# Performance work log

Measured on AMD Instinct MI355X. Metric: run time of the kernel, lower is better.

## Reference

```python
import jax, jax.numpy as jnp
from jax import lax
import numpy as np

T = 8  # num_temp_tokens (init kwarg, closed over as a static constant)


def setup_inputs() -> dict:
    key = jax.random.key(0)
    k1, k2, k3, k4, k5 = jax.random.split(key, 5)
    B, N, C = 16, 197, 768
    bt = B * T
    x = jax.random.normal(k1, (bt, N, C), dtype=jnp.float32)
    # routing conv1d: C -> 3C, kernel 3 (original inits to zero; small random for testing)
    a_weight = jax.random.normal(k2, (3 * C, C, 3), dtype=jnp.float32) * 0.02
    a_bias = jax.random.normal(k3, (3 * C,), dtype=jnp.float32) * 0.02
    # main linear weight (out_channels=3C, in_channels=C) and bias
    weight = jax.random.normal(k4, (3 * C, C), dtype=jnp.float32) * 0.02
    bias = jax.random.normal(k5, (3 * C,), dtype=jnp.float32) * 0.02
    return {"x": x, "a_weight": a_weight, "a_bias": a_bias, "weight": weight, "bias": bias}


def reference(x, a_weight, a_bias, weight, bias):
    bt, n, c = x.shape
    b = bt // T
    xr = x.reshape(b, T, n, c)                      # (b, t, n, c)
    # routing: conv1d over T on the CLS token, then +1
    cls = jnp.transpose(xr[:, :, 0, :], (0, 2, 1))  # (b, c, t)
    r = lax.conv_general_dilated(
        cls, a_weight, window_strides=(1,), padding=[(1, 1)],
        dimension_numbers=("NCH", "OIH", "NCH"),
    ) + a_bias[None, :, None] + 1.0                 # (b, 3c, t)
    s = jnp.transpose(r, (0, 2, 1)).reshape(b, T, 3, c)   # per-(b,t) q/k/v c_in scales
    Wr = weight.reshape(3, c, c)                    # (3, c_out, c_in)
    br = bias.reshape(3, c)
    # scale input channels per (b, t, group), then batched GEMM
    xs = xr[:, :, None, :, :] * s[:, :, :, None, :]       # (b, t, 3, n, c)
    out = jnp.einsum("goi,btgni->btgon", Wr, xs)          # (b, t, 3, c_out, n)
    out = out + (br[None, None] * s)[..., None]           # bias also modulated by scales
    return out.reshape(bt, 3 * c, n)                # (b*t, 3c, n) == torch output layout
```

## Files before the change

kernel.cpp:

```cpp
#include <hip/hip_runtime.h>

#define NTOK 197
#define C 768
#define C3 2304
#define BK 32
#define PK 40
#define NT 13
#define CPAD 772
#define AWP 200

typedef __attribute__((ext_vector_type(4))) float f32x4;
typedef __attribute__((ext_vector_type(8))) short bf16x8;
typedef unsigned int u32;

__device__ __forceinline__ ushort f2bf(float f){
  uint u = __float_as_uint(f);
  u += 0x7fffu + ((u >> 16) & 1u);
  return (ushort)(u >> 16);
}
__device__ __forceinline__ uint pack2(float a, float b){
  return (uint)f2bf(a) | ((uint)f2bf(b) << 16);
}
__device__ __forceinline__ float bfu2f(uint u){ return __uint_as_float(u << 16); }

__device__ __forceinline__ void glds16(ushort* lds, const ushort* gsrc){
  __builtin_amdgcn_global_load_lds((const __attribute__((address_space(1))) u32*)gsrc,
                                   (__attribute__((address_space(3))) u32*)lds, 16, 0, 0);
}

#define N4_W 442368
#define N4_X 4841472
__global__ __launch_bounds__(256)
void cvt_all(const float* __restrict__ w, const float* __restrict__ x,
             ushort* __restrict__ wbf, ushort* __restrict__ xbf)
{
  const int tid0 = blockIdx.x*256 + threadIdx.x;
  const int stride = gridDim.x*256;
  for (int i = tid0; i < N4_W; i += stride){
    float4 v = reinterpret_cast<const float4*>(w)[i];
    ushort4 o; o.x=f2bf(v.x); o.y=f2bf(v.y); o.z=f2bf(v.z); o.w=f2bf(v.w);
    reinterpret_cast<ushort4*>(wbf)[i] = o;
  }
  for (int i = tid0; i < N4_X; i += stride){
    float4 v = reinterpret_cast<const float4*>(x)[i];
    ushort4 o; o.x=f2bf(v.x); o.y=f2bf(v.y); o.z=f2bf(v.z); o.w=f2bf(v.w);
    reinterpret_cast<ushort4*>(xbf)[i] = o;
  }
}

__global__ __launch_bounds__(256)
void conv_part(const float* __restrict__ x, const float* __restrict__ aw,
               float* __restrict__ partial)
{
  __shared__ __align__(16) float  cls[16][10][68];
  __shared__ __align__(16) ushort awt[64*64*4];
  const int oc = blockIdx.x, kp = blockIdx.y, tid = threadIdx.x;
  const int k0 = kp*64;

  for (int task = tid; task < 2560; task += 256){
    int b = task / 160, rem = task % 160;
    int tp = rem / 16, c4 = rem % 16;
    float4 v = {0.f,0.f,0.f,0.f};
    if (tp >= 1 && tp <= 8)
      v = *reinterpret_cast<const float4*>(x + (size_t)(b*8 + tp - 1)*NTOK*C + k0 + c4*4);
    *reinterpret_cast<float4*>(&cls[b][tp][c4*4]) = v;
  }
  for (int task = tid; task < 1024; task += 256){
    int r = task >> 4, kc = task & 15;
    const float* p = aw + (size_t)(oc*64 + r)*2304 + (size_t)(k0 + kc*4)*3;
    float4 f0 = *reinterpret_cast<const float4*>(p);
    float4 f1 = *reinterpret_cast<const float4*>(p+4);
    float4 f2 = *reinterpret_cast<const float4*>(p+8);
    float f[12] = {f0.x,f0.y,f0.z,f0.w, f1.x,f1.y,f1.z,f1.w, f2.x,f2.y,f2.z,f2.w};
    uint4 o0, o1;
    o0.x = pack2(f[0], f[1]);  o0.y = (uint)f2bf(f[2]);
    o0.z = pack2(f[3], f[4]);  o0.w = (uint)f2bf(f[5]);
    o1.x = pack2(f[6], f[7]);  o1.y = (uint)f2bf(f[8]);
    o1.z = pack2(f[9], f[10]); o1.w = (uint)f2bf(f[11]);
    uint4* dst = reinterpret_cast<uint4*>(&awt[(r*64 + kc*4)*4]);
    dst[0] = o0; dst[1] = o1;
  }
  __syncthreads();

  const int o_l = tid >> 2, bq = tid & 3;
  float acc[8][4];
  #pragma unroll
  for (int t=0;t<8;t++)
    #pragma unroll
    for (int bi=0;bi<4;bi++) acc[t][bi]=0.f;

  #pragma unroll 1
  for (int kc = 0; kc < 16; ++kc){
    const uint4* ap = reinterpret_cast<const uint4*>(&awt[(o_l*64 + kc*4)*4]);
    uint4 aw0 = ap[0], aw1 = ap[1];
    float wv[4][3];
    wv[0][0]=bfu2f(aw0.x&0xffffu); wv[0][1]=bfu2f(aw0.x>>16); wv[0][2]=bfu2f(aw0.y&0xffffu);
    wv[1][0]=bfu2f(aw0.z&0xffffu); wv[1][1]=bfu2f(aw0.z>>16); wv[1][2]=bfu2f(aw0.w&0xffffu);
    wv[2][0]=bfu2f(aw1.x&0xffffu); wv[2][1]=bfu2f(aw1.x>>16); wv[2][2]=bfu2f(aw1.y&0xffffu);
    wv[3][0]=bfu2f(aw1.z&0xffffu); wv[3][1]=bfu2f(aw1.z>>16); wv[3][2]=bfu2f(aw1.w&0xffffu);
    #pragma unroll
    for (int bi=0; bi<4; ++bi){
      const int b = bq + 4*bi;
      float4 cv[10];
      #pragma unroll
      for (int tp=0; tp<10; tp++)
        cv[tp] = *reinterpret_cast<const float4*>(&cls[b][tp][kc*4]);
      #pragma unroll
      for (int t=0;t<8;t++){
        #pragma unroll
        for (int dk=0;dk<3;dk++){
          const float* cp = reinterpret_cast<const float*>(&cv[t+dk]);
          #pragma unroll
          for (int e=0;e<4;e++)
            acc[t][bi] += wv[e][dk] * cp[e];
        }
      }
    }
  }

  #pragma unroll
  for (int bi=0;bi<4;bi++){
    const int b = bq + 4*bi;
    #pragma unroll
    for (int t=0;t<8;t++)
      partial[((size_t)kp*128 + b*8 + t)*C3 + oc*64 + o_l] = acc[t][bi];
  }
}

__global__ __launch_bounds__(256)
void conv_reduce(const float* __restrict__ partial, const float* __restrict__ ab,
                 float* __restrict__ s_ws)
{
  const int o  = blockIdx.x*256 + threadIdx.x;
  const int bt = blockIdx.y;
  float v = ab[o] + 1.0f;
  #pragma unroll
  for (int kp=0; kp<12; kp++)
    v += partial[((size_t)kp*128 + bt)*C3 + o];
  s_ws[(size_t)bt*C3 + o] = v;
}

__global__ __launch_bounds__(256)
void gemm4(const ushort* __restrict__ wbf, const ushort* __restrict__ xbf,
           const float* __restrict__ s_ws, const float* __restrict__ bias,
           float* __restrict__ out)
{
  __shared__ __align__(16) ushort A_lds[2][128*BK];
  __shared__ __align__(16) ushort B_lds[2][208*BK];

  const int lid  = blockIdx.x;
  const int work = (lid & 7)*288 + (lid >> 3);
  const int bt   = work / 18;
  const int rem  = work - bt*18;
  const int g    = rem / 6;
  const int mt   = rem - g*6;

  const int tid = threadIdx.x, w = tid >> 6, lane = tid & 63;
  const int l15 = lane & 15, lq = lane >> 4;

  const float*  srow = s_ws + (size_t)bt*C3 + (size_t)g*C;
  const ushort* Ap   = wbf + ((size_t)g*C + (size_t)mt*128)*C;
  const ushort* xb   = xbf + (size_t)bt*NTOK*C;

  const int arow = tid >> 1;
  const int acol = (tid & 1) * 16;
  const ushort* awp = Ap + (size_t)arow*C + acol;
  const float*  asp = srow + acol;
  const int brow = lane >> 2;
  const int bcol = (lane & 3) * 8;

  f32x4 acc[2][13];
  #pragma unroll
  for (int i=0;i<2;i++)
    #pragma unroll
    for (int j=0;j<13;j++) acc[i][j] = (f32x4){0.f,0.f,0.f,0.f};

  {
    uint4 w0 = *reinterpret_cast<const uint4*>(awp);
    uint4 w1 = *reinterpret_cast<const uint4*>(awp + 8);
    float4 s0 = *reinterpret_cast<const float4*>(asp);
    float4 s1 = *reinterpret_cast<const float4*>(asp+4);
    float4 s2 = *reinterpret_cast<const float4*>(asp+8);
    float4 s3 = *reinterpret_cast<const float4*>(asp+12);
    for (int e = w; e < 13; e += 4)
      glds16(&B_lds[0][e*512], xb + (size_t)(e*16 + brow)*C + bcol);
    uint4 o0, o1;
    o0.x = pack2(bfu2f(w0.x&0xffffu)*s0.x, bfu2f(w0.x>>16)*s0.y);
    o0.y = pack2(bfu2f(w0.y&0xffffu)*s0.z, bfu2f(w0.y>>16)*s0.w);
    o0.z = pack2(bfu2f(w0.z&0xffffu)*s1.x, bfu2f(w0.z>>16)*s1.y);
    o0.w = pack2(bfu2f(w0.w&0xffffu)*s1.z, bfu2f(w0.w>>16)*s1.w);
    o1.x = pack2(bfu2f(w1.x&0xffffu)*s2.x, bfu2f(w1.x>>16)*s2.y);
    o1.y = pack2(bfu2f(w1.y&0xffffu)*s2.z, bfu2f(w1.y>>16)*s2.w);
    o1.z = pack2(bfu2f(w1.z&0xffffu)*s3.x, bfu2f(w1.z>>16)*s3.y);
    o1.w = pack2(bfu2f(w1.w&0xffffu)*s3.z, bfu2f(w1.w>>16)*s3.w);
    *reinterpret_cast<uint4*>(&A_lds[0][arow*BK + acol    ]) = o0;
    *reinterpret_cast<uint4*>(&A_lds[0][arow*BK + acol + 8]) = o1;
  }
  __syncthreads();

  for (int t = 0; t < 24; ++t){
    const int cur = t & 1, nxt = cur ^ 1;
    const int kn = t*BK + BK;
    uint4 w0, w1; float4 s0, s1, s2, s3;
    if (t < 23){
      w0 = *reinterpret_cast<const uint4*>(awp + kn);
      w1 = *reinterpret_cast<const uint4*>(awp + kn + 8);
      s0 = *reinterpret_cast<const float4*>(asp + kn);
      s1 = *reinterpret_cast<const float4*>(asp + kn + 4);
      s2 = *reinterpret_cast<const float4*>(asp + kn + 8);
      s3 = *reinterpret_cast<const float4*>(asp + kn + 12);
      for (int e = w; e < 13; e += 4)
        glds16(&B_lds[nxt][e*512], xb + (size_t)(e*16 + brow)*C + kn + bcol);
    }

    bf16x8 a0 = *reinterpret_cast<const bf16x8*>(&A_lds[cur][(w*32      + l15)*BK + lq*8]);
    bf16x8 a1 = *reinterpret_cast<const bf16x8*>(&A_lds[cur][(w*32 + 16 + l15)*BK + lq*8]);
    #pragma unroll
    for (int nf=0; nf<13; nf++){
      bf16x8 b = *reinterpret_cast<const bf16x8*>(&B_lds[cur][(nf*16 + l15)*BK + lq*8]);
      acc[0][nf] = __builtin_amdgcn_mfma_f32_16x16x32_bf16(a0, b, acc[0][nf], 0, 0, 0);
      acc[1][nf] = __builtin_amdgcn_mfma_f32_16x16x32_bf16(a1, b, acc[1][nf], 0, 0, 0);
    }

    if (t < 23){
      uint4 o0, o1;
      o0.x = pack2(bfu2f(w0.x&0xffffu)*s0.x, bfu2f(w0.x>>16)*s0.y);
      o0.y = pack2(bfu2f(w0.y&0xffffu)*s0.z, bfu2f(w0.y>>16)*s0.w);
      o0.z = pack2(bfu2f(w0.z&0xffffu)*s1.x, bfu2f(w0.z>>16)*s1.y);
      o0.w = pack2(bfu2f(w0.w&0xffffu)*s1.z, bfu2f(w0.w>>16)*s1.w);
      o1.x = pack2(bfu2f(w1.x&0xffffu)*s2.x, bfu2f(w1.x>>16)*s2.y);
      o1.y = pack2(bfu2f(w1.y&0xffffu)*s2.z, bfu2f(w1.y>>16)*s2.w);
      o1.z = pack2(bfu2f(w1.z&0xffffu)*s3.x, bfu2f(w1.z>>16)*s3.y);
      o1.w = pack2(bfu2f(w1.w&0xffffu)*s3.z, bfu2f(w1.w>>16)*s3.w);
      *reinterpret_cast<uint4*>(&A_lds[nxt][arow*BK + acol    ]) = o0;
      *reinterpret_cast<uint4*>(&A_lds[nxt][arow*BK + acol + 8]) = o1;
      __syncthreads();
    }
  }

  #pragma unroll
  for (int mf=0; mf<2; mf++){
    const int o0 = mt*128 + w*32 + mf*16 + lq*4;
    float bs[4];
    #pragma unroll
    for (int r=0;r<4;r++)
      bs[r] = bias[g*C + o0 + r] * srow[o0 + r];
    #pragma unroll
    for (int nf=0; nf<13; nf++){
      int n = nf*16 + l15;
      if (n < NTOK){
        #pragma unroll
        for (int r=0;r<4;r++)
          out[((size_t)bt*C3 + g*C + o0 + r)*NTOK + n] = acc[mf][nf][r] + bs[r];
      }
    }
  }
}

__global__ __launch_bounds__(256)
void conv3(const float* __restrict__ x, const float* __restrict__ aw,
           const float* __restrict__ ab, float* __restrict__ s_ws)
{
  __shared__ __align__(16) float  cls[10][CPAD];
  __shared__ __align__(16) ushort awt[64*AWP];
  __shared__ float partial[64][4][9];
  const int oc = blockIdx.x, b = blockIdx.y, tid = threadIdx.x;

  for (int task = tid; task < 1920; task += 256){
    int row = task / 192, c4 = task % 192;
    float4 v = {0.f,0.f,0.f,0.f};
    if (row >= 1 && row <= 8)
      v = *reinterpret_cast<const float4*>(x + (size_t)(b*8 + row - 1)*NTOK*C + c4*4);
    *reinterpret_cast<float4*>(&cls[row][c4*4]) = v;
  }

  const int o_l = tid >> 2, part = tid & 3;
  float acc[8];
  #pragma unroll
  for (int t=0;t<8;t++) acc[t]=0.f;

  for (int it = 0; it < 12; ++it){
    const int i0 = it*64;
    #pragma unroll
    for (int j = 0; j < 12; ++j){
      int task = tid + j*256;
      int r = task / 48, c4 = task % 48;
      float4 v = *reinterpret_cast<const float4*>(aw + (size_t)(oc*64 + r)*C3 + i0*3 + c4*4);
      uint2 pk; pk.x = pack2(v.x, v.y); pk.y = pack2(v.z, v.w);
      *reinterpret_cast<uint2*>(&awt[r*AWP + c4*4]) = pk;
    }
    __syncthreads();

    #pragma unroll
    for (int qq = 0; qq < 4; ++qq){
      const int i_loc = part*16 + qq*4;
      const int ib = i0 + i_loc;
      float4 cv[10];
      #pragma unroll
      for (int t=0;t<10;t++) cv[t] = *reinterpret_cast<const float4*>(&cls[t][ib]);
      float wv[4][3];
      #pragma unroll
      for (int e=0;e<4;e++){
        #pragma unroll
        for (int dk=0;dk<3;dk++)
          wv[e][dk] = bfu2f((uint)awt[o_l*AWP + (i_loc+e)*3 + dk]);
      }
      #pragma unroll
      for (int e=0;e<4;e++){
        #pragma unroll
        for (int dk=0;dk<3;dk++){
          const float wf = wv[e][dk];
          #pragma unroll
          for (int t=0;t<8;t++){
            const float* cp = reinterpret_cast<const float*>(&cv[t+dk]);
            acc[t] += wf * cp[e];
          }
        }
      }
    }
    __syncthreads();
  }

  #pragma unroll
  for (int t=0;t<8;t++) partial[o_l][part][t] = acc[t];
  __syncthreads();

  for (int idx = tid; idx < 512; idx += 256){
    int o = idx >> 3, t = idx & 7;
    float v = partial[o][0][t] + partial[o][1][t]
            + partial[o][2][t] + partial[o][3][t]
            + ab[oc*64 + o] + 1.0f;
    s_ws[(size_t)(b*8 + t)*C3 + oc*64 + o] = v;
  }
}

__global__ __launch_bounds__(512)
void gemm_fb(const float* __restrict__ x, const ushort* __restrict__ wbf,
             const float* __restrict__ s_ws, const float* __restrict__ bias,
             float* __restrict__ out)
{
  __shared__ __align__(16) ushort A_lds[128*PK];
  __shared__ __align__(16) ushort B_lds[208*PK];
  const int ot  = blockIdx.x;
  const int g   = blockIdx.y;
  const int bt  = blockIdx.z;
  const int tid = threadIdx.x;
  const int w = tid >> 6, lane = tid & 63;
  const int l15 = lane & 15, lq = lane >> 4;

  const float*  srow  = s_ws + (size_t)bt*C3 + (size_t)g*C;
  const ushort* wrow  = wbf + ((size_t)g*C + (size_t)ot*128)*C;
  const float*  xrow  = x   + (size_t)bt*NTOK*C;

  f32x4 acc[NT];
  #pragma unroll
  for (int j=0;j<NT;j++) acc[j] = (f32x4){0.f,0.f,0.f,0.f};

  const int ar = tid >> 2, ac = tid & 3;

  for (int k0 = 0; k0 < C; k0 += BK){
    {
      uint4 wv = *reinterpret_cast<const uint4*>(wrow + (size_t)ar*C + k0 + ac*8);
      const float* sv = srow + k0 + ac*8;
      float4 s0 = *reinterpret_cast<const float4*>(sv);
      float4 s1 = *reinterpret_cast<const float4*>(sv+4);
      uint4 av;
      av.x = pack2(bfu2f(wv.x & 0xffffu)*s0.x, bfu2f(wv.x >> 16)*s0.y);
      av.y = pack2(bfu2f(wv.y & 0xffffu)*s0.z, bfu2f(wv.y >> 16)*s0.w);
      av.z = pack2(bfu2f(wv.z & 0xffffu)*s1.x, bfu2f(wv.z >> 16)*s1.y);
      av.w = pack2(bfu2f(wv.w & 0xffffu)*s1.z, bfu2f(wv.w >> 16)*s1.w);
      *reinterpret_cast<uint4*>(&A_lds[ar*PK + ac*8]) = av;
    }
    #pragma unroll
    for (int it = 0; it < 2; ++it){
      int task = tid + it*512;
      if (task < 832){
        int r = task >> 2, cc = task & 3;
        uint4 bv = {0u,0u,0u,0u};
        if (r < NTOK){
          const float* p = xrow + (size_t)r*C + k0 + cc*8;
          float4 lo = *reinterpret_cast<const float4*>(p);
          float4 hi = *reinterpret_cast<const float4*>(p+4);
          bv.x = pack2(lo.x, lo.y); bv.y = pack2(lo.z, lo.w);
          bv.z = pack2(hi.x, hi.y); bv.w = pack2(hi.z, hi.w);
        }
        *reinterpret_cast<uint4*>(&B_lds[r*PK + cc*8]) = bv;
      }
    }
    __syncthreads();

    bf16x8 a = *reinterpret_cast<const bf16x8*>(&A_lds[(w*16 + l15)*PK + lq*8]);
    #pragma unroll
    for (int j=0;j<NT;j++){
      bf16x8 b = *reinterpret_cast<const bf16x8*>(&B_lds[(j*16 + l15)*PK + lq*8]);
      acc[j] = __builtin_amdgcn_mfma_f32_16x16x32_bf16(a, b, acc[j], 0, 0, 0);
    }
    __syncthreads();
  }

  const int obase = ot*128 + w*16 + lq*4;
  float bs[4];
  #pragma unroll
  for (int r=0;r<4;r++)
    bs[r] = bias[g*C + obase + r] * srow[obase + r];
  #pragma unroll
  for (int j=0;j<NT;j++){
    int n = j*16 + l15;
    if (n < NTOK){
      #pragma unroll
      for (int r=0;r<4;r++)
        out[((size_t)bt*C3 + g*C + obase + r)*NTOK + n] = acc[j][r] + bs[r];
    }
  }
}

__global__ void cvt_w_only(const float* __restrict__ in, ushort* __restrict__ outp, int n4)
{
  int stride = gridDim.x * blockDim.x;
  for (int i = blockIdx.x*blockDim.x + threadIdx.x; i < n4; i += stride){
    float4 v = reinterpret_cast<const float4*>(in)[i];
    ushort4 o;
    o.x = f2bf(v.x); o.y = f2bf(v.y); o.z = f2bf(v.z); o.w = f2bf(v.w);
    reinterpret_cast<ushort4*>(outp)[i] = o;
  }
}

extern "C" void kernel_launch(void* const* d_in, const int* in_sizes, int n_in,
                              void* d_out, int out_size, void* d_ws, size_t ws_size,
                              hipStream_t stream)
{
  const float* x        = (const float*)d_in[0];
  const float* a_weight = (const float*)d_in[1];
  const float* a_bias   = (const float*)d_in[2];
  const float* weight   = (const float*)d_in[3];
  const float* bias     = (const float*)d_in[4];
  float* out = (float*)d_out;

  char* ws = (char*)d_ws;
  float*  s_ws = (float*)ws;
  ushort* wbf  = (ushort*)(ws + 1179648);
  ushort* xbf  = (ushort*)(ws + 4718592);
  float*  part = (float*)(ws + 43450368);
  const size_t NEED_FULL = 57638912;

  if (ws_size >= NEED_FULL){
    conv_part<<<dim3(36,12), 256, 0, stream>>>(x, a_weight, part);
    conv_reduce<<<dim3(9,128), 256, 0, stream>>>(part, a_bias, s_ws);
    cvt_all<<<dim3(2048), 256, 0, stream>>>(weight, x, wbf, xbf);
    gemm4<<<dim3(2304), 256, 0, stream>>>(wbf, xbf, s_ws, bias, out);
  } else {
    cvt_w_only<<<dim3(1728), 256, 0, stream>>>(weight, wbf, 442368);
    conv3<<<dim3(36,16), 256, 0, stream>>>(x, a_weight, a_bias, s_ws);
    gemm_fb<<<dim3(6,3,128), 512, 0, stream>>>(x, wbf, s_ws, bias, out);
  }
}
```

Baseline: 491.6 us.

## Pre-scale activations per group into bf16 planes and retile GEMM to 2x2 warps

Moves the per-(b,t,group) channel scaling from the weight tile inside the GEMM loop onto the activations, written once into three padded bf16 planes by a new scale_x kernel. The weight bf16 conversion is folded into the conv reduction kernel. The GEMM now loads plain bf16 A and B tiles through registers into padded LDS and uses a 2x2 warp layout with 4x7 MFMA fragments per warp. This removes the per-iteration unpack/scale/repack work on A in exchange for writing and reading a scaled X that is three times larger, and it raises the workspace requirement.

```diff
diff --git a/kernel.cpp b/kernel.cpp
--- a/kernel.cpp
+++ b/kernel.cpp
@@ -4,10 +4,13 @@
 #define C 768
 #define C3 2304
 #define BK 32
+#define PKA 36
+#define PKB 36
 #define PK 40
 #define NT 13
 #define CPAD 772
 #define AWP 200
+#define XS_PLANE 20447232
 
 typedef __attribute__((ext_vector_type(4))) float f32x4;
 typedef __attribute__((ext_vector_type(8))) short bf16x8;
@@ -22,31 +25,6 @@
   return (uint)f2bf(a) | ((uint)f2bf(b) << 16);
 }
 __device__ __forceinline__ float bfu2f(uint u){ return __uint_as_float(u << 16); }
-
-__device__ __forceinline__ void glds16(ushort* lds, const ushort* gsrc){
-  __builtin_amdgcn_global_load_lds((const __attribute__((address_space(1))) u32*)gsrc,
-                                   (__attribute__((address_space(3))) u32*)lds, 16, 0, 0);
-}
-
-#define N4_W 442368
-#define N4_X 4841472
-__global__ __launch_bounds__(256)
-void cvt_all(const float* __restrict__ w, const float* __restrict__ x,
-             ushort* __restrict__ wbf, ushort* __restrict__ xbf)
-{
-  const int tid0 = blockIdx.x*256 + threadIdx.x;
-  const int stride = gridDim.x*256;
-  for (int i = tid0; i < N4_W; i += stride){
-    float4 v = reinterpret_cast<const float4*>(w)[i];
-    ushort4 o; o.x=f2bf(v.x); o.y=f2bf(v.y); o.z=f2bf(v.z); o.w=f2bf(v.w);
-    reinterpret_cast<ushort4*>(wbf)[i] = o;
-  }
-  for (int i = tid0; i < N4_X; i += stride){
-    float4 v = reinterpret_cast<const float4*>(x)[i];
-    ushort4 o; o.x=f2bf(v.x); o.y=f2bf(v.y); o.z=f2bf(v.z); o.w=f2bf(v.w);
-    reinterpret_cast<ushort4*>(xbf)[i] = o;
-  }
-}
 
 __global__ __launch_bounds__(256)
 void conv_part(const float* __restrict__ x, const float* __restrict__ aw,
@@ -127,9 +105,11 @@
   }
 }
 
+#define N4_W 442368
 __global__ __launch_bounds__(256)
-void conv_reduce(const float* __restrict__ partial, const float* __restrict__ ab,
-                 float* __restrict__ s_ws)
+void conv_reduce2(const float* __restrict__ partial, const float* __restrict__ ab,
+                  float* __restrict__ s_ws,
+                  const float* __restrict__ w, ushort* __restrict__ wbf)
 {
   const int o  = blockIdx.x*256 + threadIdx.x;
   const int bt = blockIdx.y;
@@ -138,15 +118,57 @@
   for (int kp=0; kp<12; kp++)
     v += partial[((size_t)kp*128 + bt)*C3 + o];
   s_ws[(size_t)bt*C3 + o] = v;
+
+  const int gtid = (blockIdx.y*9 + blockIdx.x)*256 + threadIdx.x;
+  for (int i = gtid; i < N4_W; i += 294912){
+    float4 f = reinterpret_cast<const float4*>(w)[i];
+    ushort4 u; u.x=f2bf(f.x); u.y=f2bf(f.y); u.z=f2bf(f.z); u.w=f2bf(f.w);
+    reinterpret_cast<ushort4*>(wbf)[i] = u;
+  }
 }
 
 __global__ __launch_bounds__(256)
-void gemm4(const ushort* __restrict__ wbf, const ushort* __restrict__ xbf,
+void scale_x(const float* __restrict__ x, const float* __restrict__ s_ws,
+             ushort* __restrict__ Xs)
+{
+  const int NCH = 128*208*96;
+  int stride = gridDim.x * blockDim.x;
+  for (int idx = blockIdx.x*blockDim.x + threadIdx.x; idx < NCH; idx += stride){
+    int kc = idx % 96;
+    int n  = (idx / 96) % 208;
+    int bt = idx / (96*208);
+    uint4 og[3];
+    #pragma unroll
+    for (int g=0; g<3; g++) og[g] = (uint4){0u,0u,0u,0u};
+    if (n < NTOK){
+      const float* xp = x + ((size_t)bt*NTOK + n)*C + kc*8;
+      float4 xa = *reinterpret_cast<const float4*>(xp);
+      float4 xb = *reinterpret_cast<const float4*>(xp+4);
+      #pragma unroll
+      for (int g=0; g<3; g++){
+        const float* sp = s_ws + (size_t)bt*C3 + g*C + kc*8;
+        float4 sa = *reinterpret_cast<const float4*>(sp);
+        float4 sb = *reinterpret_cast<const float4*>(sp+4);
+        og[g].x = pack2(xa.x*sa.x, xa.y*sa.y);
+        og[g].y = pack2(xa.z*sa.z, xa.w*sa.w);
+        og[g].z = pack2(xb.x*sb.x, xb.y*sb.y);
+        og[g].w = pack2(xb.z*sb.z, xb.w*sb.w);
+      }
+    }
+    size_t base = ((size_t)bt*208 + n)*C + kc*8;
+    #pragma unroll
+    for (int g=0; g<3; g++)
+      *reinterpret_cast<uint4*>(Xs + (size_t)g*XS_PLANE + base) = og[g];
+  }
+}
+
+__global__ __launch_bounds__(256, 3)
+void gemm6(const ushort* __restrict__ wbf, const ushort* __restrict__ Xs,
            const float* __restrict__ s_ws, const float* __restrict__ bias,
            float* __restrict__ out)
 {
-  __shared__ __align__(16) ushort A_lds[2][128*BK];
-  __shared__ __align__(16) ushort B_lds[2][208*BK];
+  __shared__ __align__(16) ushort A_lds[2][128*PKA];
+  __shared__ __align__(16) ushort B_lds[2][224*PKB];
 
   const int lid  = blockIdx.x;
   const int work = (lid & 7)*288 + (lid >> 3);
@@ -157,97 +179,98 @@
 
   const int tid = threadIdx.x, w = tid >> 6, lane = tid & 63;
   const int l15 = lane & 15, lq = lane >> 4;
+  const int wm = w >> 1, wn = w & 1;
 
   const float*  srow = s_ws + (size_t)bt*C3 + (size_t)g*C;
   const ushort* Ap   = wbf + ((size_t)g*C + (size_t)mt*128)*C;
-  const ushort* xb   = xbf + (size_t)bt*NTOK*C;
+  const ushort* Bp   = Xs + (size_t)g*XS_PLANE + (size_t)bt*208*C;
 
   const int arow = tid >> 1;
   const int acol = (tid & 1) * 16;
   const ushort* awp = Ap + (size_t)arow*C + acol;
-  const float*  asp = srow + acol;
-  const int brow = lane >> 2;
-  const int bcol = (lane & 3) * 8;
-
-  f32x4 acc[2][13];
-  #pragma unroll
-  for (int i=0;i<2;i++)
-    #pragma unroll
-    for (int j=0;j<13;j++) acc[i][j] = (f32x4){0.f,0.f,0.f,0.f};
+
+  const int br0 = tid >> 2,         bc = (tid & 3) * 8;
+  const int br1 = (tid + 256) >> 2;
+  const int br2 = (tid + 512) >> 2;
+  const int br3 = 192 + (tid >> 2);
 
   {
-    uint4 w0 = *reinterpret_cast<const uint4*>(awp);
-    uint4 w1 = *reinterpret_cast<const uint4*>(awp + 8);
-    float4 s0 = *reinterpret_cast<const float4*>(asp);
-    float4 s1 = *reinterpret_cast<const float4*>(asp+4);
-    float4 s2 = *reinterpret_cast<const float4*>(asp+8);
-    float4 s3 = *reinterpret_cast<const float4*>(asp+12);
-    for (int e = w; e < 13; e += 4)
-      glds16(&B_lds[0][e*512], xb + (size_t)(e*16 + brow)*C + bcol);
-    uint4 o0, o1;
-    o0.x = pack2(bfu2f(w0.x&0xffffu)*s0.x, bfu2f(w0.x>>16)*s0.y);
-    o0.y = pack2(bfu2f(w0.y&0xffffu)*s0.z, bfu2f(w0.y>>16)*s0.w);
-    o0.z = pack2(bfu2f(w0.z&0xffffu)*s1.x, bfu2f(w0.z>>16)*s1.y);
-    o0.w = pack2(bfu2f(w0.w&0xffffu)*s1.z, bfu2f(w0.w>>16)*s1.w);
-    o1.x = pack2(bfu2f(w1.x&0xffffu)*s2.x, bfu2f(w1.x>>16)*s2.y);
-    o1.y = pack2(bfu2f(w1.y&0xffffu)*s2.z, bfu2f(w1.y>>16)*s2.w);
-    o1.z = pack2(bfu2f(w1.z&0xffffu)*s3.x, bfu2f(w1.z>>16)*s3.y);
-    o1.w = pack2(bfu2f(w1.w&0xffffu)*s3.z, bfu2f(w1.w>>16)*s3.w);
-    *reinterpret_cast<uint4*>(&A_lds[0][arow*BK + acol    ]) = o0;
-    *reinterpret_cast<uint4*>(&A_lds[0][arow*BK + acol + 8]) = o1;
+    uint* p0 = reinterpret_cast<uint*>(&B_lds[0][208*PKB]);
+    uint* p1 = reinterpret_cast<uint*>(&B_lds[1][208*PKB]);
+    for (int i = tid; i < 288; i += 256){ p0[i] = 0u; p1[i] = 0u; }
+  }
+
+  f32x4 acc[4][7];
+  #pragma unroll
+  for (int i=0;i<4;i++)
+    #pragma unroll
+    for (int j=0;j<7;j++) acc[i][j] = (f32x4){0.f,0.f,0.f,0.f};
+
+  {
+    uint4 a0 = *reinterpret_cast<const uint4*>(awp);
+    uint4 a1 = *reinterpret_cast<const uint4*>(awp + 8);
+    uint4 b0 = *reinterpret_cast<const uint4*>(Bp + (size_t)br0*C + bc);
+    uint4 b1 = *reinterpret_cast<const uint4*>(Bp + (size_t)br1*C + bc);
+    uint4 b2 = *reinterpret_cast<const uint4*>(Bp + (size_t)br2*C + bc);
+    uint4 b3;
+    if (tid < 64) b3 = *reinterpret_cast<const uint4*>(Bp + (size_t)br3*C + bc);
+    *reinterpret_cast<uint4*>(&A_lds[0][arow*PKA + acol    ]) = a0;
+    *reinterpret_cast<uint4*>(&A_lds[0][arow*PKA + acol + 8]) = a1;
+    *reinterpret_cast<uint4*>(&B_lds[0][br0*PKB + bc]) = b0;
+    *reinterpret_cast<uint4*>(&B_lds[0][br1*PKB + bc]) = b1;
+    *reinterpret_cast<uint4*>(&B_lds[0][br2*PKB + bc]) = b2;
+    if (tid < 64)
+      *reinterpret_cast<uint4*>(&B_lds[0][br3*PKB + bc]) = b3;
   }
   __syncthreads();
 
   for (int t = 0; t < 24; ++t){
     const int cur = t & 1, nxt = cur ^ 1;
     const int kn = t*BK + BK;
-    uint4 w0, w1; float4 s0, s1, s2, s3;
+    uint4 a0, a1, b0, b1, b2, b3;
     if (t < 23){
-      w0 = *reinterpret_cast<const uint4*>(awp + kn);
-      w1 = *reinterpret_cast<const uint4*>(awp + kn + 8);
-      s0 = *reinterpret_cast<const float4*>(asp + kn);
-      s1 = *reinterpret_cast<const float4*>(asp + kn + 4);
-      s2 = *reinterpret_cast<const float4*>(asp + kn + 8);
-      s3 = *reinterpret_cast<const float4*>(asp + kn + 12);
-      for (int e = w; e < 13; e += 4)
-        glds16(&B_lds[nxt][e*512], xb + (size_t)(e*16 + brow)*C + kn + bcol);
-    }
-
-    bf16x8 a0 = *reinterpret_cast<const bf16x8*>(&A_lds[cur][(w*32      + l15)*BK + lq*8]);
-    bf16x8 a1 = *reinterpret_cast<const bf16x8*>(&A_lds[cur][(w*32 + 16 + l15)*BK + lq*8]);
-    #pragma unroll
-    for (int nf=0; nf<13; nf++){
-      bf16x8 b = *reinterpret_cast<const bf16x8*>(&B_lds[cur][(nf*16 + l15)*BK + lq*8]);
-      acc[0][nf] = __builtin_amdgcn_mfma_f32_16x16x32_bf16(a0, b, acc[0][nf], 0, 0, 0);
-      acc[1][nf] = __builtin_amdgcn_mfma_f32_16x16x32_bf16(a1, b, acc[1][nf], 0, 0, 0);
+      a0 = *reinterpret_cast<const uint4*>(awp + kn);
+      a1 = *reinterpret_cast<const uint4*>(awp + kn + 8);
+      b0 = *reinterpret_cast<const uint4*>(Bp + (size_t)br0*C + kn + bc);
+      b1 = *reinterpret_cast<const uint4*>(Bp + (size_t)br1*C + kn + bc);
+      b2 = *reinterpret_cast<const uint4*>(Bp + (size_t)br2*C + kn + bc);
+      if (tid < 64) b3 = *reinterpret_cast<const uint4*>(Bp + (size_t)br3*C + kn + bc);
+    }
+
+    bf16x8 af[4];
+    #pragma unroll
+    for (int mf=0; mf<4; mf++)
+      af[mf] = *reinterpret_cast<const bf16x8*>(&A_lds[cur][(wm*64 + mf*16 + l15)*PKA + lq*8]);
+    #pragma unroll
+    for (int nf=0; nf<7; nf++){
+      bf16x8 bf = *reinterpret_cast<const bf16x8*>(&B_lds[cur][((wn*7 + nf)*16 + l15)*PKB + lq*8]);
+      #pragma unroll
+      for (int mf=0; mf<4; mf++)
+        acc[mf][nf] = __builtin_amdgcn_mfma_f32_16x16x32_bf16(af[mf], bf, acc[mf][nf], 0, 0, 0);
     }
 
     if (t < 23){
-      uint4 o0, o1;
-      o0.x = pack2(bfu2f(w0.x&0xffffu)*s0.x, bfu2f(w0.x>>16)*s0.y);
-      o0.y = pack2(bfu2f(w0.y&0xffffu)*s0.z, bfu2f(w0.y>>16)*s0.w);
-      o0.z = pack2(bfu2f(w0.z&0xffffu)*s1.x, bfu2f(w0.z>>16)*s1.y);
-      o0.w = pack2(bfu2f(w0.w&0xffffu)*s1.z, bfu2f(w0.w>>16)*s1.w);
-      o1.x = pack2(bfu2f(w1.x&0xffffu)*s2.x, bfu2f(w1.x>>16)*s2.y);
-      o1.y = pack2(bfu2f(w1.y&0xffffu)*s2.z, bfu2f(w1.y>>16)*s2.w);
-      o1.z = pack2(bfu2f(w1.z&0xffffu)*s3.x, bfu2f(w1.z>>16)*s3.y);
-      o1.w = pack2(bfu2f(w1.w&0xffffu)*s3.z, bfu2f(w1.w>>16)*s3.w);
-      *reinterpret_cast<uint4*>(&A_lds[nxt][arow*BK + acol    ]) = o0;
-      *reinterpret_cast<uint4*>(&A_lds[nxt][arow*BK + acol + 8]) = o1;
+      *reinterpret_cast<uint4*>(&A_lds[nxt][arow*PKA + acol    ]) = a0;
+      *reinterpret_cast<uint4*>(&A_lds[nxt][arow*PKA + acol + 8]) = a1;
+      *reinterpret_cast<uint4*>(&B_lds[nxt][br0*PKB + bc]) = b0;
+      *reinterpret_cast<uint4*>(&B_lds[nxt][br1*PKB + bc]) = b1;
+      *reinterpret_cast<uint4*>(&B_lds[nxt][br2*PKB + bc]) = b2;
+      if (tid < 64)
+        *reinterpret_cast<uint4*>(&B_lds[nxt][br3*PKB + bc]) = b3;
       __syncthreads();
     }
   }
 
   #pragma unroll
-  for (int mf=0; mf<2; mf++){
-    const int o0 = mt*128 + w*32 + mf*16 + lq*4;
+  for (int mf=0; mf<4; mf++){
+    const int o0 = mt*128 + wm*64 + mf*16 + lq*4;
     float bs[4];
     #pragma unroll
     for (int r=0;r<4;r++)
       bs[r] = bias[g*C + o0 + r] * srow[o0 + r];
     #pragma unroll
-    for (int nf=0; nf<13; nf++){
-      int n = nf*16 + l15;
+    for (int nf=0; nf<7; nf++){
+      int n = (wn*7 + nf)*16 + l15;
       if (n < NTOK){
         #pragma unroll
         for (int r=0;r<4;r++)
@@ -439,15 +462,15 @@
   char* ws = (char*)d_ws;
   float*  s_ws = (float*)ws;
   ushort* wbf  = (ushort*)(ws + 1179648);
-  ushort* xbf  = (ushort*)(ws + 4718592);
-  float*  part = (float*)(ws + 43450368);
-  const size_t NEED_FULL = 57638912;
+  ushort* Xs   = (ushort*)(ws + 4718592);
+  float*  part = (float*)(ws + 4718592);
+  const size_t NEED_FULL = 127401984;
 
   if (ws_size >= NEED_FULL){
     conv_part<<<dim3(36,12), 256, 0, stream>>>(x, a_weight, part);
-    conv_reduce<<<dim3(9,128), 256, 0, stream>>>(part, a_bias, s_ws);
-    cvt_all<<<dim3(2048), 256, 0, stream>>>(weight, x, wbf, xbf);
-    gemm4<<<dim3(2304), 256, 0, stream>>>(wbf, xbf, s_ws, bias, out);
+    conv_reduce2<<<dim3(9,128), 256, 0, stream>>>(part, a_bias, s_ws, weight, wbf);
+    scale_x<<<dim3(2048), 256, 0, stream>>>(x, s_ws, Xs);
+    gemm6<<<dim3(2304), 256, 0, stream>>>(wbf, Xs, s_ws, bias, out);
   } else {
     cvt_w_only<<<dim3(1728), 256, 0, stream>>>(weight, wbf, 442368);
     conv3<<<dim3(36,16), 256, 0, stream>>>(x, a_weight, a_bias, s_ws);
```

After: 582.1 us. 18.4% more time.
